# Optimization experiments

Measured on AMD Instinct MI355X. Metric: run time of the kernel, lower is better.

Reference implementation:

```python
import jax, jax.numpy as jnp
import numpy as np
import math

B, S, D, H, L, V, MAXLEN = 4, 2047, 256, 8, 2, 32000, 2048
DK = D // H
DFF = 2 * D
EPS = 1e-5


def make_pe(max_len, d):
    pos = jnp.arange(max_len, dtype=jnp.float32)[:, None]
    div = jnp.exp(jnp.arange(0, d, 2, dtype=jnp.float32) * (-math.log(10000.0) / d))
    pe = jnp.zeros((max_len, d), dtype=jnp.float32)
    pe = pe.at[:, 0::2].set(jnp.sin(pos * div))
    pe = pe.at[:, 1::2].set(jnp.cos(pos * div))
    return pe[None]  # [1, max_len, d]


def setup_inputs() -> dict:
    key = jax.random.key(0)
    ks = jax.random.split(key, 16)
    s = 0.02
    T = S + 1
    return {
        "embeddings": jax.random.normal(ks[0], (B, D), jnp.float32),
        "output_tokens": jax.random.randint(ks[1], (B, S), 0, V, jnp.int64),
        "causal_mask": jnp.tril(jnp.ones((T, T), jnp.int32))[None, None],  # [1,1,T,T]
        "key_padding_mask": jnp.ones((B, 1, 1, T), jnp.int32),
        "tok_emb": jax.random.normal(ks[2], (V, D), jnp.float32) * s,
        "pe": make_pe(MAXLEN, D),
        "Wq": jax.random.normal(ks[3], (L, D, D), jnp.float32) * s,
        "Wk": jax.random.normal(ks[4], (L, D, D), jnp.float32) * s,
        "Wv": jax.random.normal(ks[5], (L, D, D), jnp.float32) * s,
        "Wo": jax.random.normal(ks[6], (L, D, D), jnp.float32) * s,
        "bo": jnp.zeros((L, D), jnp.float32),
        "ln1_g": jnp.ones((L, D), jnp.float32),
        "ln1_b": jnp.zeros((L, D), jnp.float32),
        "W1": jax.random.normal(ks[7], (L, D, DFF), jnp.float32) * s,
        "b1": jnp.zeros((L, DFF), jnp.float32),
        "W2": jax.random.normal(ks[8], (L, DFF, D), jnp.float32) * s,
        "b2": jnp.zeros((L, D), jnp.float32),
        "ln2_g": jnp.ones((L, D), jnp.float32),
        "ln2_b": jnp.zeros((L, D), jnp.float32),
    }


def layer_norm(x, g, b):
    mu = jnp.mean(x, axis=-1, keepdims=True)
    var = jnp.mean(jnp.square(x - mu), axis=-1, keepdims=True)
    return (x - mu) * jax.lax.rsqrt(var + EPS) * g + b


def attention(x, Wq, Wk, Wv, Wo, bo, causal_mask, key_padding_mask):
    b, t, d = x.shape
    q = (x @ Wq).reshape(b, t, H, DK)
    k = (x @ Wk).reshape(b, t, H, DK)
    v = (x @ Wv).reshape(b, t, H, DK)
    scores = jnp.einsum('bqhd,bkhd->bhqk', q, k) / math.sqrt(DK)  # [B,H,T,T]
    neg = jnp.float32(-jnp.inf)
    scores = jnp.where(causal_mask == 0, neg, scores)
    scores = jnp.where(key_padding_mask == 0, neg, scores)
    attn = jax.nn.softmax(scores, axis=-1)
    out = jnp.einsum('bhqk,bkhd->bqhd', attn, v).reshape(b, t, d)
    return out @ Wo + bo


def reference(embeddings, output_tokens, causal_mask, key_padding_mask,
              tok_emb, pe, Wq, Wk, Wv, Wo, bo, ln1_g, ln1_b,
              W1, b1, W2, b2, ln2_g, ln2_b):
    emb_tok = tok_emb[output_tokens]                       # [B,S,D]
    x = jnp.concatenate([embeddings[:, None, :], emb_tok], axis=1)  # [B,T,D]
    x = x + pe[:, :x.shape[1]]
    for l in range(L):
        a = attention(x, Wq[l], Wk[l], Wv[l], Wo[l], bo[l], causal_mask, key_padding_mask)
        x = layer_norm(x + a, ln1_g[l], ln1_b[l])
        ff = jax.nn.relu(x @ W1[l] + b1[l]) @ W2[l] + b2[l]
        x = layer_norm(x + ff, ln2_g[l], ln2_b[l])
    return x[:, 1:, :]  # drop the prepended embedding position
```

## Files before the change

kernel.cpp:

```cpp
#include <hip/hip_runtime.h>
#include <cstdint>
#include <cstddef>

#define B_   4
#define S_   2047
#define T_   2048
#define D_   256
#define H_   8
#define DK_  32
#define DFF_ 512
#define L_   2

typedef short          s8v  __attribute__((ext_vector_type(8)));
typedef float          f4v  __attribute__((ext_vector_type(4)));
typedef unsigned short u4v  __attribute__((ext_vector_type(4)));
typedef unsigned short u8v  __attribute__((ext_vector_type(8)));
typedef unsigned int   u2v  __attribute__((ext_vector_type(2)));
typedef unsigned int   uint32;

union U8 { u8v v; unsigned short e[8]; };

__device__ __forceinline__ float bf2f(unsigned short h) {
    unsigned int u = ((unsigned int)h) << 16;
    float f; __builtin_memcpy(&f, &u, 4); return f;
}
__device__ __forceinline__ unsigned short f2bf(float f) {
    unsigned int u; __builtin_memcpy(&u, &f, 4);
    u += 0x7fffu + ((u >> 16) & 1u);
    return (unsigned short)(u >> 16);
}
__device__ __forceinline__ uint32 pack_bf2(float lo, float hi) {
    uint32 a, b;
    __builtin_memcpy(&a, &lo, 4); __builtin_memcpy(&b, &hi, 4);
    a += 0x8000u; b += 0x8000u;
    return __builtin_amdgcn_perm(b, a, 0x07060302);
}

#define QSCALE2 0.25503485951542068f

__global__ __launch_bounds__(256) void prep_k(
    const float* __restrict__ emb, const int* __restrict__ toks,
    const float* __restrict__ tokE, const float* __restrict__ pe,
    unsigned short* __restrict__ X,
    const float* __restrict__ Wq, const float* __restrict__ Wk,
    const float* __restrict__ Wv, const float* __restrict__ Wo,
    const float* __restrict__ W1, const float* __restrict__ W2,
    unsigned short* __restrict__ WqkvT, unsigned short* __restrict__ WoT,
    unsigned short* __restrict__ W1T, unsigned short* __restrict__ W2T)
{
    __shared__ float tile[32][33];
    if (blockIdx.x < 1024) {
        int idx = blockIdx.x * 256 + threadIdx.x;
        int d8 = (idx & 31) * 8;
        int t  = (idx >> 5) & (T_ - 1);
        int b  = idx >> 16;
        const float* src = (t == 0) ? (emb + b * D_)
                                    : (tokE + (size_t)toks[b * S_ + t - 1] * D_);
        const float* p = pe + (size_t)t * D_ + d8;
        U8 o;
#pragma unroll
        for (int j = 0; j < 8; ++j) o.e[j] = f2bf(src[d8 + j] + p[j]);
        *(u8v*)(X + (size_t)(b * T_ + t) * D_ + d8) = o.v;
        return;
    }
    int idx = blockIdx.x - 1024;
    const float* src; unsigned short* dst; int R, C, tr, tc;
    if (idx < 512) {
        int w = idx >> 7, rem = idx & 127, l = rem >> 6, t = rem & 63;
        tr = t >> 3; tc = t & 7; R = 256; C = 256;
        src = (w == 0 ? Wq : w == 1 ? Wk : w == 2 ? Wv : Wo) + (size_t)l * 65536;
        dst = (w < 3) ? WqkvT + (size_t)l * 196608 + (size_t)w * 65536
                      : WoT + (size_t)l * 65536;
    } else if (idx < 768) {
        int rem = idx - 512, l = rem >> 7, t = rem & 127;
        tr = t >> 4; tc = t & 15; R = 256; C = 512;
        src = W1 + (size_t)l * 131072; dst = W1T + (size_t)l * 131072;
    } else {
        int rem = idx - 768, l = rem >> 7, t = rem & 127;
        tr = t >> 3; tc = t & 7; R = 512; C = 256;
        src = W2 + (size_t)l * 131072; dst = W2T + (size_t)l * 131072;
    }
    int x = threadIdx.x & 31, y = threadIdx.x >> 5;
    int r0 = tr * 32, c0 = tc * 32;
#pragma unroll
    for (int i = 0; i < 32; i += 8) tile[y + i][x] = src[(size_t)(r0 + y + i) * C + c0 + x];
    __syncthreads();
#pragma unroll
    for (int i = 0; i < 32; i += 8)
        dst[(size_t)(c0 + y + i) * R + r0 + x] = f2bf(tile[x][y + i]);
}

__global__ __launch_bounds__(256) void gemm64_k(
    const unsigned short* __restrict__ A, const unsigned short* __restrict__ WT,
    const float* __restrict__ bias,
    unsigned short* __restrict__ oq, unsigned short* __restrict__ ok,
    unsigned short* __restrict__ ov, unsigned short* __restrict__ out,
    int K, int Ntot, int mode)
{
    __shared__ unsigned short At[64 * 72];
    __shared__ unsigned short Wt[64 * 72];
    const int tid = threadIdx.x;
    const int wave = tid >> 6, lane = tid & 63, l15 = lane & 15, quad = lane >> 4;
    const int m0 = blockIdx.x * 64, n0g = blockIdx.y * 64;

    f4v acc[4];
#pragma unroll
    for (int i = 0; i < 4; ++i) acc[i] = (f4v){0.f, 0.f, 0.f, 0.f};

    const int arow = tid >> 2, acg = (tid & 3) * 16;
    const unsigned short* ag = A + (size_t)(m0 + arow) * K + acg;
    const unsigned short* wg = WT + (size_t)(n0g + arow) * K + acg;
    u8v a0 = *(const u8v*)ag, a1 = *(const u8v*)(ag + 8);
    u8v w0 = *(const u8v*)wg, w1 = *(const u8v*)(wg + 8);

    const int niter = K >> 6;
    for (int kk = 0; kk < niter; ++kk) {
        *(u8v*)&At[arow * 72 + acg] = a0; *(u8v*)&At[arow * 72 + acg + 8] = a1;
        *(u8v*)&Wt[arow * 72 + acg] = w0; *(u8v*)&Wt[arow * 72 + acg + 8] = w1;
        __syncthreads();
        if (kk + 1 < niter) {
            int o = (kk + 1) * 64;
            a0 = *(const u8v*)(ag + o); a1 = *(const u8v*)(ag + o + 8);
            w0 = *(const u8v*)(wg + o); w1 = *(const u8v*)(wg + o + 8);
        }
#pragma unroll
        for (int ks = 0; ks < 2; ++ks) {
            s8v aF = *(const s8v*)&At[(wave * 16 + l15) * 72 + ks * 32 + quad * 8];
#pragma unroll
            for (int nt = 0; nt < 4; ++nt) {
                s8v wF = *(const s8v*)&Wt[(nt * 16 + l15) * 72 + ks * 32 + quad * 8];
                acc[nt] = __builtin_amdgcn_mfma_f32_16x16x32_bf16(aF, wF, acc[nt], 0, 0, 0);
            }
        }
        __syncthreads();
    }

    const int b = m0 >> 11, t0 = m0 & (T_ - 1);
    if (mode == 0) {
        int sub = blockIdx.y >> 2;
        int cb  = (blockIdx.y & 3) * 64;
        if (sub < 2) {
            unsigned short* dst = sub ? ok : oq;
            float sc = sub ? 1.f : QSCALE2;
#pragma unroll
            for (int nt = 0; nt < 4; ++nt) {
                int c = cb + nt * 16 + l15, hh = c >> 5, dk = c & 31;
#pragma unroll
                for (int r = 0; r < 4; ++r) {
                    int t = t0 + wave * 16 + quad * 4 + r;
                    dst[((size_t)(b * H_ + hh) * T_ + t) * DK_ + dk] = f2bf(acc[nt][r] * sc);
                }
            }
        } else {
            unsigned short* Vb = At;
#pragma unroll
            for (int nt = 0; nt < 4; ++nt) {
                int base = (nt * 16 + l15) * 72 + wave * 16 + quad * 4;
                *(uint32*)&Vb[base]     = pack_bf2(acc[nt][0], acc[nt][1]);
                *(uint32*)&Vb[base + 2] = pack_bf2(acc[nt][2], acc[nt][3]);
            }
            __syncthreads();
            int c = tid >> 2, chunk = tid & 3;
            int cg = cb + c, hh = cg >> 5, dk = cg & 31;
            unsigned short* dst = ov + ((size_t)(b * H_ + hh) * DK_ + dk) * T_ + t0 + chunk * 16;
            u8v v0 = *(u8v*)&Vb[c * 72 + chunk * 16];
            u8v v1 = *(u8v*)&Vb[c * 72 + chunk * 16 + 8];
            *(u8v*)dst = v0; *(u8v*)(dst + 8) = v1;
        }
    } else {
#pragma unroll
        for (int nt = 0; nt < 4; ++nt) {
            int c = n0g + nt * 16 + l15;
            float bv = bias[c];
#pragma unroll
            for (int r = 0; r < 4; ++r) {
                float v = acc[nt][r] + bv;
                v = v > 0.f ? v : 0.f;
                out[(size_t)(m0 + wave * 16 + quad * 4 + r) * Ntot + c] = f2bf(v);
            }
        }
    }
}

__global__ __launch_bounds__(256) void attn_k(
    const unsigned short* __restrict__ Qh, const unsigned short* __restrict__ Kh,
    const unsigned short* __restrict__ VT, unsigned short* __restrict__ AO)
{
    __shared__ unsigned short Kt[128 * 40];
    __shared__ unsigned short Vt[32 * 144];
    __shared__ unsigned short Ps[4][16 * 136];

    const int tid = threadIdx.x, wave = tid >> 6, lane = tid & 63;
    const int l15 = lane & 15, quad = lane >> 4;
    const int bh = blockIdx.y, b = bh >> 3, h = bh & 7;
    const size_t hoff = (size_t)bh * T_ * DK_;
    unsigned short* Pw = &Ps[wave][0];

    const int qts[2] = { (int)blockIdx.x, 31 - (int)blockIdx.x };
    const int nk0 = qts[0] / 2 + 1, nk1 = qts[1] / 2 + 1;
    const int ntot = nk0 + nk1;

    const int krow = tid >> 1, khalf = (tid & 1) * 16;
    const int vdk = tid >> 3, vc = (tid & 7) * 16;
    const unsigned short* kgp = Kh + hoff + (size_t)krow * DK_ + khalf;
    const unsigned short* vgp = VT + ((size_t)bh * DK_ + vdk) * T_ + vc;

    u8v kr0 = *(const u8v*)kgp, kr1 = *(const u8v*)(kgp + 8);
    u8v vr0 = *(const u8v*)vgp, vr1 = *(const u8v*)(vgp + 8);

    s8v qB = {0,0,0,0,0,0,0,0};
    f4v O0 = {0,0,0,0}, O1 = {0,0,0,0};
    float l_i = 0.f;
    int nkt = 0, q0w = 0;

    for (int it = 0; it < ntot; ++it) {
        const int phase = (it >= nk0);
        const int kt = phase ? it - nk0 : it;
        if (kt == 0) {
            int qt = qts[phase]; nkt = phase ? nk1 : nk0;
            q0w = qt * 64 + wave * 16;
            qB = *(const s8v*)(Qh + hoff + (size_t)(q0w + l15) * DK_ + quad * 8);
            O0 = (f4v){0,0,0,0}; O1 = (f4v){0,0,0,0};
            l_i = 0.f;
        }
        *(u8v*)&Kt[krow * 40 + khalf]     = kr0;
        *(u8v*)&Kt[krow * 40 + khalf + 8] = kr1;
        *(u8v*)&Vt[vdk * 144 + vc]        = vr0;
        *(u8v*)&Vt[vdk * 144 + vc + 8]    = vr1;
        __syncthreads();
        {
            int itn = it + 1;
            if (itn < ntot) {
                int ktn = (itn >= nk0) ? itn - nk0 : itn;
                const unsigned short* kn = kgp + (size_t)ktn * 128 * DK_;
                const unsigned short* vn = vgp + (size_t)ktn * 128;
                kr0 = *(const u8v*)kn; kr1 = *(const u8v*)(kn + 8);
                vr0 = *(const u8v*)vn; vr1 = *(const u8v*)(vn + 8);
            }
        }
        const int k0 = kt * 128;

        f4v s[8];
        f4v zero = {0,0,0,0};
#pragma unroll
        for (int nt = 0; nt < 8; ++nt) {
            s8v kA = *(const s8v*)&Kt[(nt * 16 + l15) * 40 + quad * 8];
            s[nt] = __builtin_amdgcn_mfma_f32_16x16x32_bf16(kA, qB, zero, 0, 0, 0);
        }
        if (kt == nkt - 1) {
            int query = q0w + l15;
#pragma unroll
            for (int nt = 0; nt < 8; ++nt)
#pragma unroll
                for (int r = 0; r < 4; ++r) {
                    int key = k0 + nt * 16 + quad * 4 + r;
                    if (key > query) s[nt][r] = -1e30f;
                }
        }
        float rs = 0.f;
#pragma unroll
        for (int nt = 0; nt < 8; ++nt)
#pragma unroll
            for (int r = 0; r < 4; ++r) {
                float p = exp2f(s[nt][r]);
                s[nt][r] = p;
                rs += p;
            }
        rs += __shfl_xor(rs, 16);
        rs += __shfl_xor(rs, 32);
        l_i += rs;
#pragma unroll
        for (int nt = 0; nt < 8; ++nt) {
            u2v pw;
            pw.x = pack_bf2(s[nt][0], s[nt][1]);
            pw.y = pack_bf2(s[nt][2], s[nt][3]);
            *(u2v*)&Pw[l15 * 136 + nt * 16 + quad * 4] = pw;
        }
#pragma unroll
        for (int ks = 0; ks < 4; ++ks) {
            s8v aP = *(const s8v*)&Pw[l15 * 136 + ks * 32 + quad * 8];
            s8v v0 = *(const s8v*)&Vt[l15 * 144 + ks * 32 + quad * 8];
            s8v v1 = *(const s8v*)&Vt[(16 + l15) * 144 + ks * 32 + quad * 8];
            O0 = __builtin_amdgcn_mfma_f32_16x16x32_bf16(aP, v0, O0, 0, 0, 0);
            O1 = __builtin_amdgcn_mfma_f32_16x16x32_bf16(aP, v1, O1, 0, 0, 0);
        }
        if (kt == nkt - 1) {
#pragma unroll
            for (int r = 0; r < 4; ++r) {
                float linv = 1.f / __shfl(l_i, quad * 4 + r);
                int row = q0w + quad * 4 + r;
                size_t base = (size_t)(b * T_ + row) * D_ + h * DK_;
                AO[base + l15]      = f2bf(O0[r] * linv);
                AO[base + 16 + l15] = f2bf(O1[r] * linv);
            }
        }
        __syncthreads();
    }
}

template<int K>
__device__ __forceinline__ void ldw8(s8v* dst, const unsigned short* bp, int koff) {
#pragma unroll
    for (int nt = 0; nt < 4; ++nt)
#pragma unroll
        for (int ks = 0; ks < 2; ++ks)
            dst[nt * 2 + ks] = *(const s8v*)(bp + (size_t)nt * 16 * K + koff + ks * 32);
}

__global__ __launch_bounds__(256) void tail_k(
    const unsigned short* __restrict__ AO,
    const unsigned short* __restrict__ WoTl, const float* __restrict__ bo,
    unsigned short* __restrict__ X,
    const float* __restrict__ g1, const float* __restrict__ be1,
    const unsigned short* __restrict__ W1Tl, const float* __restrict__ b1,
    const unsigned short* __restrict__ W2Tl, const float* __restrict__ b2,
    const float* __restrict__ g2, const float* __restrict__ be2,
    float* __restrict__ fout, int last)
{
    __shared__ unsigned short X1s[16 * 264];
    __shared__ unsigned short Hs[16 * 520];
    __shared__ float LNsc[128];

    const int tid = threadIdx.x;
    const int wave = tid >> 6, lane = tid & 63, l15 = lane & 15, quad = lane >> 4;
    const int m0 = blockIdx.x * 16;
    const int rbase = quad * 4;

    const unsigned short* w0p = WoTl + (size_t)(wave * 64 + l15) * 256 + quad * 8;
    const unsigned short* w1p = W1Tl + (size_t)(wave * 64 + l15) * 256 + quad * 8;
    const unsigned short* w1q = W1Tl + (size_t)(256 + wave * 64 + l15) * 256 + quad * 8;
    const unsigned short* w2p = W2Tl + (size_t)(wave * 64 + l15) * 512 + quad * 8;
    const unsigned short* a0p = AO + (size_t)(m0 + l15) * 256 + quad * 8;

    f4v acc[4];
    s8v wb[2][8];
    s8v ab[2][2];

#pragma unroll
    for (int i = 0; i < 4; ++i) acc[i] = (f4v){0.f, 0.f, 0.f, 0.f};
    ldw8<256>(&wb[0][0], w0p, 0);
    ab[0][0] = *(const s8v*)(a0p);
    ab[0][1] = *(const s8v*)(a0p + 32);
#pragma unroll
    for (int kk = 0; kk < 4; ++kk) {
        const int cur = kk & 1, nxt = cur ^ 1;
        if (kk < 3) {
            ldw8<256>(&wb[nxt][0], w0p, (kk + 1) * 64);
            ab[nxt][0] = *(const s8v*)(a0p + (kk + 1) * 64);
            ab[nxt][1] = *(const s8v*)(a0p + (kk + 1) * 64 + 32);
        } else {
            ldw8<256>(&wb[nxt][0], w1p, 0);
        }
#pragma unroll
        for (int ks = 0; ks < 2; ++ks) {
            s8v aF = ab[cur][ks];
#pragma unroll
            for (int nt = 0; nt < 4; ++nt)
                acc[nt] = __builtin_amdgcn_mfma_f32_16x16x32_bf16(aF, wb[cur][nt * 2 + ks], acc[nt], 0, 0, 0);
        }
    }
    {
        float ps[4] = {0,0,0,0}, pq[4] = {0,0,0,0};
#pragma unroll
        for (int nt = 0; nt < 4; ++nt) {
            int c = wave * 64 + nt * 16 + l15;
            float bv = bo[c];
#pragma unroll
            for (int r = 0; r < 4; ++r) {
                float v = acc[nt][r] + bv + bf2f(X[(size_t)(m0 + rbase + r) * D_ + c]);
                acc[nt][r] = v; ps[r] += v; pq[r] += v * v;
            }
        }
#pragma unroll
        for (int r = 0; r < 4; ++r) {
            float s = ps[r], q = pq[r];
            s += __shfl_xor(s, 1); q += __shfl_xor(q, 1);
            s += __shfl_xor(s, 2); q += __shfl_xor(q, 2);
            s += __shfl_xor(s, 4); q += __shfl_xor(q, 4);
            s += __shfl_xor(s, 8); q += __shfl_xor(q, 8);
            if (l15 == 0) { LNsc[(rbase + r) * 4 + wave] = s; LNsc[64 + (rbase + r) * 4 + wave] = q; }
        }
        __syncthreads();
        float mu[4], rsig[4];
#pragma unroll
        for (int r = 0; r < 4; ++r) {
            int row = rbase + r;
            float s = LNsc[row * 4] + LNsc[row * 4 + 1] + LNsc[row * 4 + 2] + LNsc[row * 4 + 3];
            float q = LNsc[64 + row * 4] + LNsc[64 + row * 4 + 1] + LNsc[64 + row * 4 + 2] + LNsc[64 + row * 4 + 3];
            float m = s * (1.f / 256.f);
            mu[r] = m;
            rsig[r] = rsqrtf(q * (1.f / 256.f) - m * m + 1e-5f);
        }
#pragma unroll
        for (int nt = 0; nt < 4; ++nt) {
            int c = wave * 64 + nt * 16 + l15;
            float g = g1[c], be = be1[c];
#pragma unroll
            for (int r = 0; r < 4; ++r)
                X1s[(rbase + r) * 264 + c] = f2bf((acc[nt][r] - mu[r]) * rsig[r] * g + be);
        }
        __syncthreads();
    }

#pragma unroll
    for (int i = 0; i < 4; ++i) acc[i] = (f4v){0.f, 0.f, 0.f, 0.f};
#pragma unroll
    for (int kk = 0; kk < 4; ++kk) {
        const int cur = kk & 1, nxt = cur ^ 1;
        if (kk < 3) ldw8<256>(&wb[nxt][0], w1p, (kk + 1) * 64);
        else        ldw8<256>(&wb[nxt][0], w1q, 0);
#pragma unroll
        for (int ks = 0; ks < 2; ++ks) {
            s8v aF = *(const s8v*)&X1s[l15 * 264 + kk * 64 + ks * 32 + quad * 8];
#pragma unroll
            for (int nt = 0; nt < 4; ++nt)
                acc[nt] = __builtin_amdgcn_mfma_f32_16x16x32_bf16(aF, wb[cur][nt * 2 + ks], acc[nt], 0, 0, 0);
        }
    }
#pragma unroll
    for (int nt = 0; nt < 4; ++nt) {
        int c = wave * 64 + nt * 16 + l15;
        float bv = b1[c];
#pragma unroll
        for (int r = 0; r < 4; ++r) {
            float v = acc[nt][r] + bv; v = v > 0.f ? v : 0.f;
            Hs[(rbase + r) * 520 + c] = f2bf(v);
        }
    }

#pragma unroll
    for (int i = 0; i < 4; ++i) acc[i] = (f4v){0.f, 0.f, 0.f, 0.f};
#pragma unroll
    for (int kk = 0; kk < 4; ++kk) {
        const int cur = kk & 1, nxt = cur ^ 1;
        if (kk < 3) ldw8<256>(&wb[nxt][0], w1q, (kk + 1) * 64);
        else        ldw8<512>(&wb[nxt][0], w2p, 0);
#pragma unroll
        for (int ks = 0; ks < 2; ++ks) {
            s8v aF = *(const s8v*)&X1s[l15 * 264 + kk * 64 + ks * 32 + quad * 8];
#pragma unroll
            for (int nt = 0; nt < 4; ++nt)
                acc[nt] = __builtin_amdgcn_mfma_f32_16x16x32_bf16(aF, wb[cur][nt * 2 + ks], acc[nt], 0, 0, 0);
        }
    }
#pragma unroll
    for (int nt = 0; nt < 4; ++nt) {
        int c = wave * 64 + nt * 16 + l15;
        float bv = b1[256 + c];
#pragma unroll
        for (int r = 0; r < 4; ++r) {
            float v = acc[nt][r] + bv; v = v > 0.f ? v : 0.f;
            Hs[(rbase + r) * 520 + 256 + c] = f2bf(v);
        }
    }
    __syncthreads();

#pragma unroll
    for (int i = 0; i < 4; ++i) acc[i] = (f4v){0.f, 0.f, 0.f, 0.f};
#pragma unroll
    for (int kk = 0; kk < 8; ++kk) {
        const int cur = kk & 1, nxt = cur ^ 1;
        if (kk < 7) ldw8<512>(&wb[nxt][0], w2p, (kk + 1) * 64);
#pragma unroll
        for (int ks = 0; ks < 2; ++ks) {
            s8v aF = *(const s8v*)&Hs[l15 * 520 + kk * 64 + ks * 32 + quad * 8];
#pragma unroll
            for (int nt = 0; nt < 4; ++nt)
                acc[nt] = __builtin_amdgcn_mfma_f32_16x16x32_bf16(aF, wb[cur][nt * 2 + ks], acc[nt], 0, 0, 0);
        }
    }
    {
        float ps[4] = {0,0,0,0}, pq[4] = {0,0,0,0};
#pragma unroll
        for (int nt = 0; nt < 4; ++nt) {
            int c = wave * 64 + nt * 16 + l15;
            float bv = b2[c];
#pragma unroll
            for (int r = 0; r < 4; ++r) {
                float v = acc[nt][r] + bv + bf2f(X1s[(rbase + r) * 264 + c]);
                acc[nt][r] = v; ps[r] += v; pq[r] += v * v;
            }
        }
#pragma unroll
        for (int r = 0; r < 4; ++r) {
            float s = ps[r], q = pq[r];
            s += __shfl_xor(s, 1); q += __shfl_xor(q, 1);
            s += __shfl_xor(s, 2); q += __shfl_xor(q, 2);
            s += __shfl_xor(s, 4); q += __shfl_xor(q, 4);
            s += __shfl_xor(s, 8); q += __shfl_xor(q, 8);
            if (l15 == 0) { LNsc[(rbase + r) * 4 + wave] = s; LNsc[64 + (rbase + r) * 4 + wave] = q; }
        }
        __syncthreads();
        float mu[4], rsig[4];
#pragma unroll
        for (int r = 0; r < 4; ++r) {
            int row = rbase + r;
            float s = LNsc[row * 4] + LNsc[row * 4 + 1] + LNsc[row * 4 + 2] + LNsc[row * 4 + 3];
            float q = LNsc[64 + row * 4] + LNsc[64 + row * 4 + 1] + LNsc[64 + row * 4 + 2] + LNsc[64 + row * 4 + 3];
            float m = s * (1.f / 256.f);
            mu[r] = m;
            rsig[r] = rsqrtf(q * (1.f / 256.f) - m * m + 1e-5f);
        }
#pragma unroll
        for (int nt = 0; nt < 4; ++nt) {
            int c = wave * 64 + nt * 16 + l15;
            float g = g2[c], be = be2[c];
#pragma unroll
            for (int r = 0; r < 4; ++r) {
                float val = (acc[nt][r] - mu[r]) * rsig[r] * g + be;
                if (!last) {
                    X[(size_t)(m0 + rbase + r) * D_ + c] = f2bf(val);
                } else {
                    int gr = m0 + rbase + r;
                    int t = gr & (T_ - 1), bb = gr >> 11;
                    if (t) fout[((size_t)bb * S_ + t - 1) * D_ + c] = val;
                }
            }
        }
    }
}

extern "C" void kernel_launch(void* const* d_in, const int* in_sizes, int n_in,
                              void* d_out, int out_size, void* d_ws, size_t ws_size,
                              hipStream_t stream)
{
    const float* emb  = (const float*)d_in[0];
    const int*   toks = (const int*)d_in[1];
    const float* tokE = (const float*)d_in[4];
    const float* pe   = (const float*)d_in[5];
    const float* Wq   = (const float*)d_in[6];
    const float* Wk   = (const float*)d_in[7];
    const float* Wv   = (const float*)d_in[8];
    const float* Wo   = (const float*)d_in[9];
    const float* bo   = (const float*)d_in[10];
    const float* g1   = (const float*)d_in[11];
    const float* be1  = (const float*)d_in[12];
    const float* W1   = (const float*)d_in[13];
    const float* b1   = (const float*)d_in[14];
    const float* W2   = (const float*)d_in[15];
    const float* b2   = (const float*)d_in[16];
    const float* g2   = (const float*)d_in[17];
    const float* be2  = (const float*)d_in[18];
    float* out = (float*)d_out;

    unsigned short* ws = (unsigned short*)d_ws;
    size_t off = 0;
    const size_t XSZ = (size_t)B_ * T_ * D_;
    unsigned short* Xa    = ws + off; off += XSZ;
    unsigned short* Xb    = ws + off; off += XSZ;
    unsigned short* Qh    = ws + off; off += XSZ;
    unsigned short* Kh    = ws + off; off += XSZ;
    unsigned short* VTb   = ws + off; off += XSZ;
    unsigned short* AOb   = ws + off; off += XSZ;
    unsigned short* Hb    = ws + off; off += (size_t)B_ * T_ * DFF_;
    unsigned short* WqkvT = ws + off; off += (size_t)L_ * 3 * D_ * D_;
    unsigned short* WoT   = ws + off; off += (size_t)L_ * D_ * D_;
    unsigned short* W1T   = ws + off; off += (size_t)L_ * D_ * DFF_;
    unsigned short* W2T   = ws + off; off += (size_t)L_ * DFF_ * D_;
    (void)ws_size; (void)in_sizes; (void)n_in; (void)out_size;
    (void)Xb; (void)Hb;

    prep_k<<<dim3(2048), 256, 0, stream>>>(emb, toks, tokE, pe, Xa,
                                           Wq, Wk, Wv, Wo, W1, W2,
                                           WqkvT, WoT, W1T, W2T);

    for (int l = 0; l < L_; ++l) {
        const unsigned short* wqkv = WqkvT + (size_t)l * 3 * D_ * D_;
        const unsigned short* wo   = WoT + (size_t)l * D_ * D_;
        const unsigned short* w1   = W1T + (size_t)l * D_ * DFF_;
        const unsigned short* w2   = W2T + (size_t)l * DFF_ * D_;

        gemm64_k<<<dim3(128, 12), 256, 0, stream>>>(Xa, wqkv, nullptr,
                                                    Qh, Kh, VTb, nullptr, D_, D_, 0);
        attn_k<<<dim3(16, 32), 256, 0, stream>>>(Qh, Kh, VTb, AOb);
        tail_k<<<dim3(512), 256, 0, stream>>>(AOb, wo, bo + l * D_, Xa,
                                              g1 + l * D_, be1 + l * D_,
                                              w1, b1 + l * DFF_,
                                              w2, b2 + l * D_,
                                              g2 + l * D_, be2 + l * D_,
                                              out, l == L_ - 1);
    }
}
```

Baseline: 291.8 us.

## Stage FFN weights in LDS for 32-row tail blocks; double-buffer attention K/V

The fused out-projection/LayerNorm/FFN tail kernel changes from 16-row blocks of 4 waves, where each wave loaded its weights straight from global memory into registers, to 32-row blocks of 8 waves. Each 64-wide weight K-chunk is now staged once in LDS with register prefetch and shared by both row groups. This halves the number of blocks that each stream the full weight set, at the cost of more barriers and a larger LDS footprint. Separately, the attention kernel double-buffers its K/V LDS tiles, widens the V row padding, and drops the trailing per-iteration barrier, removing one sync per key tile.

```diff
diff --git a/kernel.cpp b/kernel.cpp
--- a/kernel.cpp
+++ b/kernel.cpp
@@ -182,12 +182,236 @@
     }
 }
 
+__global__ __launch_bounds__(512) void tail32_k(
+    const unsigned short* __restrict__ AO,
+    const unsigned short* __restrict__ WoTl, const float* __restrict__ bo,
+    const unsigned short* __restrict__ Xres,
+    const float* __restrict__ g1, const float* __restrict__ be1,
+    const unsigned short* __restrict__ W1Tl, const float* __restrict__ b1,
+    const unsigned short* __restrict__ W2Tl, const float* __restrict__ b2,
+    const float* __restrict__ g2, const float* __restrict__ be2,
+    unsigned short* __restrict__ Xout, float* __restrict__ fout, int last)
+{
+    __shared__ unsigned short Wt[256 * 72];
+    __shared__ unsigned short As[32 * 72];
+    __shared__ unsigned short X1s[32 * 264];
+    __shared__ unsigned short Hs[32 * 520];
+    __shared__ float LNsc[256];
+
+    const int tid = threadIdx.x;
+    const int wave = tid >> 6, lane = tid & 63, l15 = lane & 15, quad = lane >> 4;
+    const int wr = wave >> 2, wc = wave & 3;
+    const int m0 = blockIdx.x * 32;
+    const int rbase = wr * 16 + quad * 4;
+
+    const int wrow = tid >> 1, wcol = (tid & 1) * 32;
+    const int arow = tid >> 3, acol = (tid & 7) * 8;
+
+    f4v acc[4];
+    u8v w0, w1, w2, w3, a0 = {0,0,0,0,0,0,0,0};
+
+    const unsigned short* wgo = WoTl + (size_t)wrow * 256 + wcol;
+    const unsigned short* wg1 = W1Tl + (size_t)wrow * 256 + wcol;
+    const unsigned short* wg1b = W1Tl + (size_t)(256 + wrow) * 256 + wcol;
+    const unsigned short* wg2 = W2Tl + (size_t)wrow * 512 + wcol;
+    const unsigned short* ag  = AO + (size_t)(m0 + arow) * 256 + acol;
+
+#define LDW(p, o) { w0 = *(const u8v*)((p)+(o)); w1 = *(const u8v*)((p)+(o)+8); \
+                    w2 = *(const u8v*)((p)+(o)+16); w3 = *(const u8v*)((p)+(o)+24); }
+#define STW { *(u8v*)&Wt[wrow*72+wcol] = w0; *(u8v*)&Wt[wrow*72+wcol+8] = w1; \
+              *(u8v*)&Wt[wrow*72+wcol+16] = w2; *(u8v*)&Wt[wrow*72+wcol+24] = w3; }
+
+#pragma unroll
+    for (int i = 0; i < 4; ++i) acc[i] = (f4v){0.f, 0.f, 0.f, 0.f};
+    LDW(wgo, 0);
+    if (tid < 256) a0 = *(const u8v*)ag;
+    for (int kk = 0; kk < 4; ++kk) {
+        STW;
+        if (tid < 256) *(u8v*)&As[arow * 72 + acol] = a0;
+        __syncthreads();
+        if (kk < 3) {
+            LDW(wgo, (kk + 1) * 64);
+            if (tid < 256) a0 = *(const u8v*)(ag + (kk + 1) * 64);
+        } else {
+            LDW(wg1, 0);
+        }
+#pragma unroll
+        for (int ks = 0; ks < 2; ++ks) {
+            s8v aF = *(const s8v*)&As[(wr * 16 + l15) * 72 + ks * 32 + quad * 8];
+#pragma unroll
+            for (int nt = 0; nt < 4; ++nt) {
+                s8v wF = *(const s8v*)&Wt[(wc * 64 + nt * 16 + l15) * 72 + ks * 32 + quad * 8];
+                acc[nt] = __builtin_amdgcn_mfma_f32_16x16x32_bf16(aF, wF, acc[nt], 0, 0, 0);
+            }
+        }
+        __syncthreads();
+    }
+    {
+        float ps[4] = {0,0,0,0}, pq[4] = {0,0,0,0};
+#pragma unroll
+        for (int nt = 0; nt < 4; ++nt) {
+            int c = wc * 64 + nt * 16 + l15;
+            float bv = bo[c];
+#pragma unroll
+            for (int r = 0; r < 4; ++r) {
+                float v = acc[nt][r] + bv + bf2f(Xres[(size_t)(m0 + rbase + r) * D_ + c]);
+                acc[nt][r] = v; ps[r] += v; pq[r] += v * v;
+            }
+        }
+#pragma unroll
+        for (int r = 0; r < 4; ++r) {
+            float s = ps[r], q = pq[r];
+            s += __shfl_xor(s, 1); q += __shfl_xor(q, 1);
+            s += __shfl_xor(s, 2); q += __shfl_xor(q, 2);
+            s += __shfl_xor(s, 4); q += __shfl_xor(q, 4);
+            s += __shfl_xor(s, 8); q += __shfl_xor(q, 8);
+            if (l15 == 0) { LNsc[(rbase + r) * 4 + wc] = s; LNsc[128 + (rbase + r) * 4 + wc] = q; }
+        }
+        __syncthreads();
+#pragma unroll
+        for (int r = 0; r < 4; ++r) {
+            int row = rbase + r;
+            float s = LNsc[row * 4] + LNsc[row * 4 + 1] + LNsc[row * 4 + 2] + LNsc[row * 4 + 3];
+            float q = LNsc[128 + row * 4] + LNsc[128 + row * 4 + 1] + LNsc[128 + row * 4 + 2] + LNsc[128 + row * 4 + 3];
+            float m = s * (1.f / 256.f);
+            float rs = rsqrtf(q * (1.f / 256.f) - m * m + 1e-5f);
+#pragma unroll
+            for (int nt = 0; nt < 4; ++nt) {
+                int c = wc * 64 + nt * 16 + l15;
+                X1s[row * 264 + c] = f2bf((acc[nt][r] - m) * rs * g1[c] + be1[c]);
+            }
+        }
+        __syncthreads();
+    }
+
+#pragma unroll
+    for (int i = 0; i < 4; ++i) acc[i] = (f4v){0.f, 0.f, 0.f, 0.f};
+    for (int kk = 0; kk < 4; ++kk) {
+        STW;
+        __syncthreads();
+        if (kk < 3) LDW(wg1, (kk + 1) * 64) else LDW(wg1b, 0);
+#pragma unroll
+        for (int ks = 0; ks < 2; ++ks) {
+            s8v aF = *(const s8v*)&X1s[(wr * 16 + l15) * 264 + kk * 64 + ks * 32 + quad * 8];
+#pragma unroll
+            for (int nt = 0; nt < 4; ++nt) {
+                s8v wF = *(const s8v*)&Wt[(wc * 64 + nt * 16 + l15) * 72 + ks * 32 + quad * 8];
+                acc[nt] = __builtin_amdgcn_mfma_f32_16x16x32_bf16(aF, wF, acc[nt], 0, 0, 0);
+            }
+        }
+        __syncthreads();
+    }
+#pragma unroll
+    for (int nt = 0; nt < 4; ++nt) {
+        int c = wc * 64 + nt * 16 + l15;
+        float bv = b1[c];
+#pragma unroll
+        for (int r = 0; r < 4; ++r) {
+            float v = acc[nt][r] + bv; v = v > 0.f ? v : 0.f;
+            Hs[(rbase + r) * 520 + c] = f2bf(v);
+        }
+    }
+
+#pragma unroll
+    for (int i = 0; i < 4; ++i) acc[i] = (f4v){0.f, 0.f, 0.f, 0.f};
+    for (int kk = 0; kk < 4; ++kk) {
+        STW;
+        __syncthreads();
+        if (kk < 3) LDW(wg1b, (kk + 1) * 64) else LDW(wg2, 0);
+#pragma unroll
+        for (int ks = 0; ks < 2; ++ks) {
+            s8v aF = *(const s8v*)&X1s[(wr * 16 + l15) * 264 + kk * 64 + ks * 32 + quad * 8];
+#pragma unroll
+            for (int nt = 0; nt < 4; ++nt) {
+                s8v wF = *(const s8v*)&Wt[(wc * 64 + nt * 16 + l15) * 72 + ks * 32 + quad * 8];
+                acc[nt] = __builtin_amdgcn_mfma_f32_16x16x32_bf16(aF, wF, acc[nt], 0, 0, 0);
+            }
+        }
+        __syncthreads();
+    }
+#pragma unroll
+    for (int nt = 0; nt < 4; ++nt) {
+        int c = wc * 64 + nt * 16 + l15;
+        float bv = b1[256 + c];
+#pragma unroll
+        for (int r = 0; r < 4; ++r) {
+            float v = acc[nt][r] + bv; v = v > 0.f ? v : 0.f;
+            Hs[(rbase + r) * 520 + 256 + c] = f2bf(v);
+        }
+    }
+
+#pragma unroll
+    for (int i = 0; i < 4; ++i) acc[i] = (f4v){0.f, 0.f, 0.f, 0.f};
+    for (int kk = 0; kk < 8; ++kk) {
+        STW;
+        __syncthreads();
+        if (kk < 7) LDW(wg2, (kk + 1) * 64);
+#pragma unroll
+        for (int ks = 0; ks < 2; ++ks) {
+            s8v aF = *(const s8v*)&Hs[(wr * 16 + l15) * 520 + kk * 64 + ks * 32 + quad * 8];
+#pragma unroll
+            for (int nt = 0; nt < 4; ++nt) {
+                s8v wF = *(const s8v*)&Wt[(wc * 64 + nt * 16 + l15) * 72 + ks * 32 + quad * 8];
+                acc[nt] = __builtin_amdgcn_mfma_f32_16x16x32_bf16(aF, wF, acc[nt], 0, 0, 0);
+            }
+        }
+        __syncthreads();
+    }
+    {
+        float ps[4] = {0,0,0,0}, pq[4] = {0,0,0,0};
+#pragma unroll
+        for (int nt = 0; nt < 4; ++nt) {
+            int c = wc * 64 + nt * 16 + l15;
+            float bv = b2[c];
+#pragma unroll
+            for (int r = 0; r < 4; ++r) {
+                float v = acc[nt][r] + bv + bf2f(X1s[(rbase + r) * 264 + c]);
+                acc[nt][r] = v; ps[r] += v; pq[r] += v * v;
+            }
+        }
+#pragma unroll
+        for (int r = 0; r < 4; ++r) {
+            float s = ps[r], q = pq[r];
+            s += __shfl_xor(s, 1); q += __shfl_xor(q, 1);
+            s += __shfl_xor(s, 2); q += __shfl_xor(q, 2);
+            s += __shfl_xor(s, 4); q += __shfl_xor(q, 4);
+            s += __shfl_xor(s, 8); q += __shfl_xor(q, 8);
+            if (l15 == 0) { LNsc[(rbase + r) * 4 + wc] = s; LNsc[128 + (rbase + r) * 4 + wc] = q; }
+        }
+        __syncthreads();
+#pragma unroll
+        for (int r = 0; r < 4; ++r) {
+            int row = rbase + r;
+            float s = LNsc[row * 4] + LNsc[row * 4 + 1] + LNsc[row * 4 + 2] + LNsc[row * 4 + 3];
+            float q = LNsc[128 + row * 4] + LNsc[128 + row * 4 + 1] + LNsc[128 + row * 4 + 2] + LNsc[128 + row * 4 + 3];
+            float m = s * (1.f / 256.f);
+            float rs = rsqrtf(q * (1.f / 256.f) - m * m + 1e-5f);
+#pragma unroll
+            for (int nt = 0; nt < 4; ++nt) {
+                int c = wc * 64 + nt * 16 + l15;
+                float val = (acc[nt][r] - m) * rs * g2[c] + be2[c];
+                if (!last) {
+                    Xout[(size_t)(m0 + row) * D_ + c] = f2bf(val);
+                } else {
+                    int gr = m0 + row;
+                    int t = gr & (T_ - 1), bb = gr >> 11;
+                    if (t) fout[((size_t)bb * S_ + t - 1) * D_ + c] = val;
+                }
+            }
+        }
+    }
+#undef LDW
+#undef STW
+}
+
+#define KTP 5120
+#define VTP 4864
 __global__ __launch_bounds__(256) void attn_k(
     const unsigned short* __restrict__ Qh, const unsigned short* __restrict__ Kh,
     const unsigned short* __restrict__ VT, unsigned short* __restrict__ AO)
 {
-    __shared__ unsigned short Kt[128 * 40];
-    __shared__ unsigned short Vt[32 * 144];
+    __shared__ unsigned short Kt[2 * KTP];
+    __shared__ unsigned short Vt[2 * VTP];
     __shared__ unsigned short Ps[4][16 * 136];
 
     const int tid = threadIdx.x, wave = tid >> 6, lane = tid & 63;
@@ -216,6 +440,8 @@
     for (int it = 0; it < ntot; ++it) {
         const int phase = (it >= nk0);
         const int kt = phase ? it - nk0 : it;
+        unsigned short* Ktb = Kt + (it & 1) * KTP;
+        unsigned short* Vtb = Vt + (it & 1) * VTP;
         if (kt == 0) {
             int qt = qts[phase]; nkt = phase ? nk1 : nk0;
             q0w = qt * 64 + wave * 16;
@@ -223,10 +449,10 @@
             O0 = (f4v){0,0,0,0}; O1 = (f4v){0,0,0,0};
             l_i = 0.f;
         }
-        *(u8v*)&Kt[krow * 40 + khalf]     = kr0;
-        *(u8v*)&Kt[krow * 40 + khalf + 8] = kr1;
-        *(u8v*)&Vt[vdk * 144 + vc]        = vr0;
-        *(u8v*)&Vt[vdk * 144 + vc + 8]    = vr1;
+        *(u8v*)&Ktb[krow * 40 + khalf]     = kr0;
+        *(u8v*)&Ktb[krow * 40 + khalf + 8] = kr1;
+        *(u8v*)&Vtb[vdk * 152 + vc]        = vr0;
+        *(u8v*)&Vtb[vdk * 152 + vc + 8]    = vr1;
         __syncthreads();
         {
             int itn = it + 1;
@@ -244,7 +470,7 @@
         f4v zero = {0,0,0,0};
 #pragma unroll
         for (int nt = 0; nt < 8; ++nt) {
-            s8v kA = *(const s8v*)&Kt[(nt * 16 + l15) * 40 + quad * 8];
+            s8v kA = *(const s8v*)&Ktb[(nt * 16 + l15) * 40 + quad * 8];
             s[nt] = __builtin_amdgcn_mfma_f32_16x16x32_bf16(kA, qB, zero, 0, 0, 0);
         }
         if (kt == nkt - 1) {
@@ -279,8 +505,8 @@
 #pragma unroll
         for (int ks = 0; ks < 4; ++ks) {
             s8v aP = *(const s8v*)&Pw[l15 * 136 + ks * 32 + quad * 8];
-            s8v v0 = *(const s8v*)&Vt[l15 * 144 + ks * 32 + quad * 8];
-            s8v v1 = *(const s8v*)&Vt[(16 + l15) * 144 + ks * 32 + quad * 8];
+            s8v v0 = *(const s8v*)&Vtb[l15 * 152 + ks * 32 + quad * 8];
+            s8v v1 = *(const s8v*)&Vtb[(16 + l15) * 152 + ks * 32 + quad * 8];
             O0 = __builtin_amdgcn_mfma_f32_16x16x32_bf16(aP, v0, O0, 0, 0, 0);
             O1 = __builtin_amdgcn_mfma_f32_16x16x32_bf16(aP, v1, O1, 0, 0, 0);
         }
@@ -292,229 +518,6 @@
                 size_t base = (size_t)(b * T_ + row) * D_ + h * DK_;
                 AO[base + l15]      = f2bf(O0[r] * linv);
                 AO[base + 16 + l15] = f2bf(O1[r] * linv);
-            }
-        }
-        __syncthreads();
-    }
-}
-
-template<int K>
-__device__ __forceinline__ void ldw8(s8v* dst, const unsigned short* bp, int koff) {
-#pragma unroll
-    for (int nt = 0; nt < 4; ++nt)
-#pragma unroll
-        for (int ks = 0; ks < 2; ++ks)
-            dst[nt * 2 + ks] = *(const s8v*)(bp + (size_t)nt * 16 * K + koff + ks * 32);
-}
-
-__global__ __launch_bounds__(256) void tail_k(
-    const unsigned short* __restrict__ AO,
-    const unsigned short* __restrict__ WoTl, const float* __restrict__ bo,
-    unsigned short* __restrict__ X,
-    const float* __restrict__ g1, const float* __restrict__ be1,
-    const unsigned short* __restrict__ W1Tl, const float* __restrict__ b1,
-    const unsigned short* __restrict__ W2Tl, const float* __restrict__ b2,
-    const float* __restrict__ g2, const float* __restrict__ be2,
-    float* __restrict__ fout, int last)
-{
-    __shared__ unsigned short X1s[16 * 264];
-    __shared__ unsigned short Hs[16 * 520];
-    __shared__ float LNsc[128];
-
-    const int tid = threadIdx.x;
-    const int wave = tid >> 6, lane = tid & 63, l15 = lane & 15, quad = lane >> 4;
-    const int m0 = blockIdx.x * 16;
-    const int rbase = quad * 4;
-
-    const unsigned short* w0p = WoTl + (size_t)(wave * 64 + l15) * 256 + quad * 8;
-    const unsigned short* w1p = W1Tl + (size_t)(wave * 64 + l15) * 256 + quad * 8;
-    const unsigned short* w1q = W1Tl + (size_t)(256 + wave * 64 + l15) * 256 + quad * 8;
-    const unsigned short* w2p = W2Tl + (size_t)(wave * 64 + l15) * 512 + quad * 8;
-    const unsigned short* a0p = AO + (size_t)(m0 + l15) * 256 + quad * 8;
-
-    f4v acc[4];
-    s8v wb[2][8];
-    s8v ab[2][2];
-
-#pragma unroll
-    for (int i = 0; i < 4; ++i) acc[i] = (f4v){0.f, 0.f, 0.f, 0.f};
-    ldw8<256>(&wb[0][0], w0p, 0);
-    ab[0][0] = *(const s8v*)(a0p);
-    ab[0][1] = *(const s8v*)(a0p + 32);
-#pragma unroll
-    for (int kk = 0; kk < 4; ++kk) {
-        const int cur = kk & 1, nxt = cur ^ 1;
-        if (kk < 3) {
-            ldw8<256>(&wb[nxt][0], w0p, (kk + 1) * 64);
-            ab[nxt][0] = *(const s8v*)(a0p + (kk + 1) * 64);
-            ab[nxt][1] = *(const s8v*)(a0p + (kk + 1) * 64 + 32);
-        } else {
-            ldw8<256>(&wb[nxt][0], w1p, 0);
-        }
-#pragma unroll
-        for (int ks = 0; ks < 2; ++ks) {
-            s8v aF = ab[cur][ks];
-#pragma unroll
-            for (int nt = 0; nt < 4; ++nt)
-                acc[nt] = __builtin_amdgcn_mfma_f32_16x16x32_bf16(aF, wb[cur][nt * 2 + ks], acc[nt], 0, 0, 0);
-        }
-    }
-    {
-        float ps[4] = {0,0,0,0}, pq[4] = {0,0,0,0};
-#pragma unroll
-        for (int nt = 0; nt < 4; ++nt) {
-            int c = wave * 64 + nt * 16 + l15;
-            float bv = bo[c];
-#pragma unroll
-            for (int r = 0; r < 4; ++r) {
-                float v = acc[nt][r] + bv + bf2f(X[(size_t)(m0 + rbase + r) * D_ + c]);
-                acc[nt][r] = v; ps[r] += v; pq[r] += v * v;
-            }
-        }
-#pragma unroll
-        for (int r = 0; r < 4; ++r) {
-            float s = ps[r], q = pq[r];
-            s += __shfl_xor(s, 1); q += __shfl_xor(q, 1);
-            s += __shfl_xor(s, 2); q += __shfl_xor(q, 2);
-            s += __shfl_xor(s, 4); q += __shfl_xor(q, 4);
-            s += __shfl_xor(s, 8); q += __shfl_xor(q, 8);
-            if (l15 == 0) { LNsc[(rbase + r) * 4 + wave] = s; LNsc[64 + (rbase + r) * 4 + wave] = q; }
-        }
-        __syncthreads();
-        float mu[4], rsig[4];
-#pragma unroll
-        for (int r = 0; r < 4; ++r) {
-            int row = rbase + r;
-            float s = LNsc[row * 4] + LNsc[row * 4 + 1] + LNsc[row * 4 + 2] + LNsc[row * 4 + 3];
-            float q = LNsc[64 + row * 4] + LNsc[64 + row * 4 + 1] + LNsc[64 + row * 4 + 2] + LNsc[64 + row * 4 + 3];
-            float m = s * (1.f / 256.f);
-            mu[r] = m;
-            rsig[r] = rsqrtf(q * (1.f / 256.f) - m * m + 1e-5f);
-        }
-#pragma unroll
-        for (int nt = 0; nt < 4; ++nt) {
-            int c = wave * 64 + nt * 16 + l15;
-            float g = g1[c], be = be1[c];
-#pragma unroll
-            for (int r = 0; r < 4; ++r)
-                X1s[(rbase + r) * 264 + c] = f2bf((acc[nt][r] - mu[r]) * rsig[r] * g + be);
-        }
-        __syncthreads();
-    }
-
-#pragma unroll
-    for (int i = 0; i < 4; ++i) acc[i] = (f4v){0.f, 0.f, 0.f, 0.f};
-#pragma unroll
-    for (int kk = 0; kk < 4; ++kk) {
-        const int cur = kk & 1, nxt = cur ^ 1;
-        if (kk < 3) ldw8<256>(&wb[nxt][0], w1p, (kk + 1) * 64);
-        else        ldw8<256>(&wb[nxt][0], w1q, 0);
-#pragma unroll
-        for (int ks = 0; ks < 2; ++ks) {
-            s8v aF = *(const s8v*)&X1s[l15 * 264 + kk * 64 + ks * 32 + quad * 8];
-#pragma unroll
-            for (int nt = 0; nt < 4; ++nt)
-                acc[nt] = __builtin_amdgcn_mfma_f32_16x16x32_bf16(aF, wb[cur][nt * 2 + ks], acc[nt], 0, 0, 0);
-        }
-    }
-#pragma unroll
-    for (int nt = 0; nt < 4; ++nt) {
-        int c = wave * 64 + nt * 16 + l15;
-        float bv = b1[c];
-#pragma unroll
-        for (int r = 0; r < 4; ++r) {
-            float v = acc[nt][r] + bv; v = v > 0.f ? v : 0.f;
-            Hs[(rbase + r) * 520 + c] = f2bf(v);
-        }
-    }
-
-#pragma unroll
-    for (int i = 0; i < 4; ++i) acc[i] = (f4v){0.f, 0.f, 0.f, 0.f};
-#pragma unroll
-    for (int kk = 0; kk < 4; ++kk) {
-        const int cur = kk & 1, nxt = cur ^ 1;
-        if (kk < 3) ldw8<256>(&wb[nxt][0], w1q, (kk + 1) * 64);
-        else        ldw8<512>(&wb[nxt][0], w2p, 0);
-#pragma unroll
-        for (int ks = 0; ks < 2; ++ks) {
-            s8v aF = *(const s8v*)&X1s[l15 * 264 + kk * 64 + ks * 32 + quad * 8];
-#pragma unroll
-            for (int nt = 0; nt < 4; ++nt)
-                acc[nt] = __builtin_amdgcn_mfma_f32_16x16x32_bf16(aF, wb[cur][nt * 2 + ks], acc[nt], 0, 0, 0);
-        }
-    }
-#pragma unroll
-    for (int nt = 0; nt < 4; ++nt) {
-        int c = wave * 64 + nt * 16 + l15;
-        float bv = b1[256 + c];
-#pragma unroll
-        for (int r = 0; r < 4; ++r) {
-            float v = acc[nt][r] + bv; v = v > 0.f ? v : 0.f;
-            Hs[(rbase + r) * 520 + 256 + c] = f2bf(v);
-        }
-    }
-    __syncthreads();
-
-#pragma unroll
-    for (int i = 0; i < 4; ++i) acc[i] = (f4v){0.f, 0.f, 0.f, 0.f};
-#pragma unroll
-    for (int kk = 0; kk < 8; ++kk) {
-        const int cur = kk & 1, nxt = cur ^ 1;
-        if (kk < 7) ldw8<512>(&wb[nxt][0], w2p, (kk + 1) * 64);
-#pragma unroll
-        for (int ks = 0; ks < 2; ++ks) {
-            s8v aF = *(const s8v*)&Hs[l15 * 520 + kk * 64 + ks * 32 + quad * 8];
-#pragma unroll
-            for (int nt = 0; nt < 4; ++nt)
-                acc[nt] = __builtin_amdgcn_mfma_f32_16x16x32_bf16(aF, wb[cur][nt * 2 + ks], acc[nt], 0, 0, 0);
-        }
-    }
-    {
-        float ps[4] = {0,0,0,0}, pq[4] = {0,0,0,0};
-#pragma unroll
-        for (int nt = 0; nt < 4; ++nt) {
-            int c = wave * 64 + nt * 16 + l15;
-            float bv = b2[c];
-#pragma unroll
-            for (int r = 0; r < 4; ++r) {
-                float v = acc[nt][r] + bv + bf2f(X1s[(rbase + r) * 264 + c]);
-                acc[nt][r] = v; ps[r] += v; pq[r] += v * v;
-            }
-        }
-#pragma unroll
-        for (int r = 0; r < 4; ++r) {
-            float s = ps[r], q = pq[r];
-            s += __shfl_xor(s, 1); q += __shfl_xor(q, 1);
-            s += __shfl_xor(s, 2); q += __shfl_xor(q, 2);
-            s += __shfl_xor(s, 4); q += __shfl_xor(q, 4);
-            s += __shfl_xor(s, 8); q += __shfl_xor(q, 8);
-            if (l15 == 0) { LNsc[(rbase + r) * 4 + wave] = s; LNsc[64 + (rbase + r) * 4 + wave] = q; }
-        }
-        __syncthreads();
-        float mu[4], rsig[4];
-#pragma unroll
-        for (int r = 0; r < 4; ++r) {
-            int row = rbase + r;
-            float s = LNsc[row * 4] + LNsc[row * 4 + 1] + LNsc[row * 4 + 2] + LNsc[row * 4 + 3];
-            float q = LNsc[64 + row * 4] + LNsc[64 + row * 4 + 1] + LNsc[64 + row * 4 + 2] + LNsc[64 + row * 4 + 3];
-            float m = s * (1.f / 256.f);
-            mu[r] = m;
-            rsig[r] = rsqrtf(q * (1.f / 256.f) - m * m + 1e-5f);
-        }
-#pragma unroll
-        for (int nt = 0; nt < 4; ++nt) {
-            int c = wave * 64 + nt * 16 + l15;
-            float g = g2[c], be = be2[c];
-#pragma unroll
-            for (int r = 0; r < 4; ++r) {
-                float val = (acc[nt][r] - mu[r]) * rsig[r] * g + be;
-                if (!last) {
-                    X[(size_t)(m0 + rbase + r) * D_ + c] = f2bf(val);
-                } else {
-                    int gr = m0 + rbase + r;
-                    int t = gr & (T_ - 1), bb = gr >> 11;
-                    if (t) fout[((size_t)bb * S_ + t - 1) * D_ + c] = val;
-                }
             }
         }
     }
@@ -569,15 +572,16 @@
         const unsigned short* wo   = WoT + (size_t)l * D_ * D_;
         const unsigned short* w1   = W1T + (size_t)l * D_ * DFF_;
         const unsigned short* w2   = W2T + (size_t)l * DFF_ * D_;
+        const int last = (l == L_ - 1);
 
         gemm64_k<<<dim3(128, 12), 256, 0, stream>>>(Xa, wqkv, nullptr,
                                                     Qh, Kh, VTb, nullptr, D_, D_, 0);
         attn_k<<<dim3(16, 32), 256, 0, stream>>>(Qh, Kh, VTb, AOb);
-        tail_k<<<dim3(512), 256, 0, stream>>>(AOb, wo, bo + l * D_, Xa,
-                                              g1 + l * D_, be1 + l * D_,
-                                              w1, b1 + l * DFF_,
-                                              w2, b2 + l * D_,
-                                              g2 + l * D_, be2 + l * D_,
-                                              out, l == L_ - 1);
-    }
-}
+        tail32_k<<<dim3(256), 512, 0, stream>>>(AOb, wo, bo + l * D_, Xa,
+                                                g1 + l * D_, be1 + l * D_,
+                                                w1, b1 + l * DFF_,
+                                                w2, b2 + l * D_,
+                                                g2 + l * D_, be2 + l * D_,
+                                                Xa, out, last);
+    }
+}
```

Result: faster. 260.0 us (-10.9%).
